# Kernel tuning notes

Hardware: AMD Instinct MI355X
Metric: run time of the kernel (lower is better)

## Reference

```python
import jax, jax.numpy as jnp
import numpy as np

B, N, D, H = 8, 1024, 512, 512  # batch, nodes/graph, input dim, hidden/output dim
NEG_SLOPE = 0.2


def _gatv2_layer(x, src, dst, Wl, bl, Wr, br, a, bias, nseg):
    """PyG GATv2Conv (heads=1, add_self_loops=False, eval mode -> no dropout).
    message j->i: alpha_ij = softmax_i( a . leaky_relu(xl[j] + xr[i]) ); out[i] = sum_j alpha_ij * xl[j] + bias
    """
    xl = x @ Wl + bl              # [nseg, H] source transform
    xr = x @ Wr + br              # [nseg, H] target transform
    e = jax.nn.leaky_relu(xl[src] + xr[dst], NEG_SLOPE) @ a  # [E] raw scores
    m = jax.lax.stop_gradient(jax.ops.segment_max(e, dst, num_segments=nseg))
    ex = jnp.exp(e - m[dst])
    s = jax.ops.segment_sum(ex, dst, num_segments=nseg)
    alpha = ex / s[dst]                                       # segment softmax over incoming edges
    out = jax.ops.segment_sum(alpha[:, None] * xl[src], dst, num_segments=nseg)
    return out + bias


def setup_inputs() -> dict:
    key = jax.random.key(0)
    rng = np.random.RandomState(0)
    # random per-graph adjacency, avg degree ~16; block-diagonal edge extraction
    adj_np = (rng.rand(B, N, N) < (16.0 / N))
    srcs, dsts = [], []
    for b in range(B):  # matches torch.nonzero(big_adj).t(): row=src, col=dst
        r, c = np.nonzero(adj_np[b])
        srcs.append(r + b * N)
        dsts.append(c + b * N)
    edge_index = jnp.asarray(np.stack([np.concatenate(srcs), np.concatenate(dsts)]).astype(np.int32))

    ks = jax.random.split(key, 32)
    def lin(k, fi, fo):
        return (jax.random.normal(k, (fi, fo), jnp.float32) / np.sqrt(fi)).astype(jnp.float32)
    inp = {
        "batch_graph": jax.random.normal(ks[0], (B, N, D), jnp.float32),
        "adj": jnp.asarray(adj_np.astype(np.float32)),
        "edge_index": edge_index,
    }
    dims = [(D, H), (H, H), (H, H)]
    for i, (fi, fo) in enumerate(dims, start=1):
        k = jax.random.split(ks[i], 6)
        inp[f"Wl{i}"] = lin(k[0], fi, fo)
        inp[f"bl{i}"] = jnp.zeros((fo,), jnp.float32)
        inp[f"Wr{i}"] = lin(k[1], fi, fo)
        inp[f"br{i}"] = jnp.zeros((fo,), jnp.float32)
        inp[f"a{i}"] = (jax.random.normal(k[2], (fo,), jnp.float32) / np.sqrt(fo)).astype(jnp.float32)
        inp[f"bias{i}"] = jnp.zeros((fo,), jnp.float32)
    return inp


def reference(batch_graph, adj, edge_index,
              Wl1, bl1, Wr1, br1, a1, bias1,
              Wl2, bl2, Wr2, br2, a2, bias2,
              Wl3, bl3, Wr3, br3, a3, bias3):
    b, n, d = batch_graph.shape
    nseg = b * n
    x = batch_graph.reshape(nseg, d)
    src, dst = edge_index[0], edge_index[1]
    x = _gatv2_layer(x, src, dst, Wl1, bl1, Wr1, br1, a1, bias1, nseg)  # graph_norm = Identity
    x = _gatv2_layer(x, src, dst, Wl2, bl2, Wr2, br2, a2, bias2, nseg)
    x = _gatv2_layer(x, src, dst, Wl3, bl3, Wr3, br3, a3, bias3, nseg)
    return x.reshape(b, n, -1)
```

## Files before the change

kernel.cpp:

```cpp
#include <hip/hip_runtime.h>
#include <math.h>

#define MTOT 8192
#define HD   512

typedef __attribute__((ext_vector_type(8))) short bf16x8;
typedef __attribute__((ext_vector_type(4))) float floatx4;

__device__ inline unsigned short f2bf(float f) {
    unsigned int u = __float_as_uint(f);
    unsigned int r = (u + 0x7FFFu + ((u >> 16) & 1u)) >> 16;
    return (unsigned short)r;
}
__device__ inline float bf2f(unsigned short h) {
    return __uint_as_float(((unsigned int)h) << 16);
}

__device__ inline float wave_sum64(float v) {
    int t;
    t = __builtin_amdgcn_update_dpp(0, __float_as_int(v), 0x121, 0xF, 0xF, true); v += __int_as_float(t);
    t = __builtin_amdgcn_update_dpp(0, __float_as_int(v), 0x122, 0xF, 0xF, true); v += __int_as_float(t);
    t = __builtin_amdgcn_update_dpp(0, __float_as_int(v), 0x124, 0xF, 0xF, true); v += __int_as_float(t);
    t = __builtin_amdgcn_update_dpp(0, __float_as_int(v), 0x128, 0xF, 0xF, true); v += __int_as_float(t);
    v += __shfl_xor(v, 16, 64);
    v += __shfl_xor(v, 32, 64);
    return v;
}


__global__ void count_deg(const int* __restrict__ dst, int* __restrict__ deg, int E) {
    int i = blockIdx.x * 256 + threadIdx.x;
    if (i < E) atomicAdd(&deg[dst[i]], 1);
}

__global__ __launch_bounds__(1024) void scan_offsets(const int* __restrict__ deg,
                                                     int* __restrict__ offs,
                                                     int* __restrict__ cursor) {
    __shared__ int part[1024];
    int tid = threadIdx.x;
    int base = tid * 8;
    int v[8]; int s = 0;
    #pragma unroll
    for (int i = 0; i < 8; ++i) { v[i] = deg[base + i]; s += v[i]; }
    part[tid] = s;
    __syncthreads();
    for (int off = 1; off < 1024; off <<= 1) {
        int t = (tid >= off) ? part[tid - off] : 0;
        __syncthreads();
        part[tid] += t;
        __syncthreads();
    }
    int run = (tid == 0) ? 0 : part[tid - 1];
    #pragma unroll
    for (int i = 0; i < 8; ++i) {
        offs[base + i] = run;
        cursor[base + i] = run;
        run += v[i];
    }
    if (tid == 1023) offs[MTOT] = run;
}

__global__ void scatter_edges(const int* __restrict__ src, const int* __restrict__ dst,
                              int* __restrict__ cursor, int* __restrict__ csr_src, int E) {
    int i = blockIdx.x * 256 + threadIdx.x;
    if (i < E) {
        int p = atomicAdd(&cursor[dst[i]], 1);
        csr_src[p] = src[i];
    }
}


__global__ __launch_bounds__(256) void prep_convert(
    const float* __restrict__ W0, const float* __restrict__ W1,
    const float* __restrict__ W2, const float* __restrict__ W3,
    const float* __restrict__ W4, const float* __restrict__ W5,
    unsigned short* __restrict__ wtbase,
    const float* __restrict__ X,
    unsigned short* __restrict__ Ahi, unsigned short* __restrict__ Alo,
    int* __restrict__ deg)
{
    int z = blockIdx.z;
    if (z == 7) {
        if (blockIdx.x == 0 && blockIdx.y == 0)
            for (int i = threadIdx.x; i < MTOT; i += 256) deg[i] = 0;
        return;
    }
    if (z == 6) {
        int bid = blockIdx.x * 16 + blockIdx.y;
        int t0 = bid * 256 + threadIdx.x;
        #pragma unroll
        for (int it = 0; it < 16; ++it) {
            int i = (t0 + it * 65536) * 4;
            float4 vv = *(const float4*)(X + i);
            ushort4 h, l;
            h.x = f2bf(vv.x); l.x = f2bf(vv.x - bf2f(h.x));
            h.y = f2bf(vv.y); l.y = f2bf(vv.y - bf2f(h.y));
            h.z = f2bf(vv.z); l.z = f2bf(vv.z - bf2f(h.z));
            h.w = f2bf(vv.w); l.w = f2bf(vv.w - bf2f(h.w));
            *(ushort4*)(Ahi + i) = h;
            *(ushort4*)(Alo + i) = l;
        }
        return;
    }
    const float* W = (z == 0) ? W0 : (z == 1) ? W1 : (z == 2) ? W2
                   : (z == 3) ? W3 : (z == 4) ? W4 : W5;
    int L = z >> 1, lr = z & 1;
    const size_t SZ = (size_t)HD * HD;
    unsigned short* Whi = wtbase + (L * 4 + lr * 2) * SZ;
    unsigned short* Wlo = Whi + SZ;

    __shared__ float t[32][33];
    int bx = blockIdx.x * 32;
    int by = blockIdx.y * 32;
    int tx = threadIdx.x & 31, ty = threadIdx.x >> 5;
    for (int i = ty; i < 32; i += 8)
        t[i][tx] = W[(size_t)(by + i) * HD + bx + tx];
    __syncthreads();
    for (int i = ty; i < 32; i += 8) {
        float vv = t[tx][i];
        unsigned short h = f2bf(vv);
        unsigned short l = f2bf(vv - bf2f(h));
        Whi[(size_t)(bx + i) * HD + by + tx] = h;
        Wlo[(size_t)(bx + i) * HD + by + tx] = l;
    }
}


__global__ __launch_bounds__(256) void gemm_mfma_dual(
    const unsigned short* __restrict__ Ahi, const unsigned short* __restrict__ Alo,
    const unsigned short* __restrict__ Bhi_l, const unsigned short* __restrict__ Blo_l,
    const unsigned short* __restrict__ Bhi_r, const unsigned short* __restrict__ Blo_r,
    const float* __restrict__ bias_l, const float* __restrict__ bias_r,
    float* __restrict__ Cl, float* __restrict__ Cr)
{
    int bid = blockIdx.x;
    int virt = (bid & 7) * 64 + (bid >> 3);
    int g  = virt >> 3;
    int q  = virt & 7;
    int bz = q >> 2;
    int bm = g * 128, bn = (q & 3) * 128;

    const unsigned short* Bhi = bz ? Bhi_r : Bhi_l;
    const unsigned short* Blo = bz ? Blo_r : Blo_l;
    const float* bias         = bz ? bias_r : bias_l;
    float* C                  = bz ? Cr : Cl;

    __shared__ __align__(16) unsigned short lds[4 * 128 * 32];

    int tid = threadIdx.x;
    int wave = tid >> 6, lane = tid & 63;

    const unsigned short* gsrc[4] = {Ahi, Alo, Bhi, Blo};
    int rowbase[4] = {bm, bm, bn, bn};

    const unsigned short* gbase =
        gsrc[wave] + (size_t)(rowbase[wave] + (lane >> 2)) * 512 + (lane & 3) * 8;

    floatx4 acc[4][4] = {};

    int wm = wave & 1, wn = wave >> 1;
    int lr = lane & 15, lq = lane >> 4;

    for (int k0 = 0; k0 < 512; k0 += 32) {
        const unsigned short* g2 = gbase + k0;
        #pragma unroll
        for (int rg = 0; rg < 8; ++rg) {
            __builtin_amdgcn_global_load_lds(
                (const __attribute__((address_space(1))) unsigned int*)(g2 + (size_t)rg * 16 * 512),
                (__attribute__((address_space(3))) unsigned int*)(&lds[wave * 4096 + rg * 512]),
                16, 0, 0);
        }
        __syncthreads();

        bf16x8 ah[4], al[4], bh[4], bl_[4];
        #pragma unroll
        for (int i = 0; i < 4; ++i) {
            int mrow = wm * 64 + i * 16 + lr;
            ah[i]  = *(const bf16x8*)&lds[0 * 4096 + mrow * 32 + lq * 8];
            al[i]  = *(const bf16x8*)&lds[1 * 4096 + mrow * 32 + lq * 8];
            int nrow = wn * 64 + i * 16 + lr;
            bh[i]  = *(const bf16x8*)&lds[2 * 4096 + nrow * 32 + lq * 8];
            bl_[i] = *(const bf16x8*)&lds[3 * 4096 + nrow * 32 + lq * 8];
        }
        #pragma unroll
        for (int i = 0; i < 4; ++i)
            #pragma unroll
            for (int j = 0; j < 4; ++j) {
                acc[i][j] = __builtin_amdgcn_mfma_f32_16x16x32_bf16(ah[i], bh[j],  acc[i][j], 0, 0, 0);
                acc[i][j] = __builtin_amdgcn_mfma_f32_16x16x32_bf16(ah[i], bl_[j], acc[i][j], 0, 0, 0);
                acc[i][j] = __builtin_amdgcn_mfma_f32_16x16x32_bf16(al[i], bh[j],  acc[i][j], 0, 0, 0);
            }
        __syncthreads();
    }

    #pragma unroll
    for (int j = 0; j < 4; ++j) {
        int n = bn + wn * 64 + j * 16 + lr;
        float bv = bias[n];
        #pragma unroll
        for (int i = 0; i < 4; ++i) {
            int mbase = bm + wm * 64 + i * 16 + lq * 4;
            #pragma unroll
            for (int r = 0; r < 4; ++r)
                C[(size_t)(mbase + r) * 512 + n] = acc[i][j][r] + bv;
        }
    }
}


__global__ __launch_bounds__(256, 4) void gat_online(
    const float* __restrict__ xl, const float* __restrict__ xr,
    const float* __restrict__ avec, const float* __restrict__ bias,
    const int* __restrict__ offs, const int* __restrict__ csr_src,
    float* __restrict__ out, unsigned short* __restrict__ Ohi,
    unsigned short* __restrict__ Olo, int write_fp32)
{
    int gid = blockIdx.x;
    int wv = threadIdx.x >> 6, lane = threadIdx.x & 63;
    int node = ((gid & 7) << 10) + ((gid >> 3) << 2) + wv;

    int nb = offs[node], ne = offs[node + 1];

    int jc[8];
    int j0 = (nb < ne) ? csr_src[nb] : 0;
    jc[0] = j0;
    #pragma unroll
    for (int k = 1; k < 8; ++k)
        jc[k] = (nb + k < ne) ? csr_src[nb + k] : j0;

    size_t rowoff = (size_t)node * HD + lane * 8;
    float4 r0 = *(const float4*)(xr + rowoff);
    float4 r1 = *(const float4*)(xr + rowoff + 4);
    float4 av0 = *(const float4*)(avec + lane * 8);
    float4 av1 = *(const float4*)(avec + lane * 8 + 4);

    float m = -3.0e38f, s = 0.f;
    float4 acc0 = {0.f, 0.f, 0.f, 0.f}, acc1 = {0.f, 0.f, 0.f, 0.f};

    int p = nb;
    while (p < ne) {
        float4 xa[8], xb[8];
        #pragma unroll
        for (int k = 0; k < 8; ++k) {
            const float* xp = xl + (size_t)jc[k] * HD + lane * 8;
            xa[k] = *(const float4*)xp;
            xb[k] = *(const float4*)(xp + 4);
        }

        int pn = p + 8;
        int jn[8];
        #pragma unroll
        for (int k = 0; k < 8; ++k)
            jn[k] = (pn + k < ne) ? csr_src[pn + k] : jc[0];

        float pe[8];
        #pragma unroll
        for (int k = 0; k < 8; ++k) {
            float t, d = 0.f;
            t = xa[k].x + r0.x; d = fmaf(av0.x, fmaf(0.4f, fabsf(t), 0.6f * t), d);
            t = xa[k].y + r0.y; d = fmaf(av0.y, fmaf(0.4f, fabsf(t), 0.6f * t), d);
            t = xa[k].z + r0.z; d = fmaf(av0.z, fmaf(0.4f, fabsf(t), 0.6f * t), d);
            t = xa[k].w + r0.w; d = fmaf(av0.w, fmaf(0.4f, fabsf(t), 0.6f * t), d);
            t = xb[k].x + r1.x; d = fmaf(av1.x, fmaf(0.4f, fabsf(t), 0.6f * t), d);
            t = xb[k].y + r1.y; d = fmaf(av1.y, fmaf(0.4f, fabsf(t), 0.6f * t), d);
            t = xb[k].z + r1.z; d = fmaf(av1.z, fmaf(0.4f, fabsf(t), 0.6f * t), d);
            t = xb[k].w + r1.w; d = fmaf(av1.w, fmaf(0.4f, fabsf(t), 0.6f * t), d);
            pe[k] = d;
        }

        #pragma unroll
        for (int k = 0; k < 8; ++k) pe[k] = wave_sum64(pe[k]);

        float e[8];
        #pragma unroll
        for (int k = 0; k < 8; ++k) e[k] = (p + k < ne) ? pe[k] : -3.0e38f;

        float bm8 = e[0];
        #pragma unroll
        for (int k = 1; k < 8; ++k) bm8 = fmaxf(bm8, e[k]);

        if (bm8 > m) {
            float sc = __expf(m - bm8);
            s *= sc;
            acc0.x *= sc; acc0.y *= sc; acc0.z *= sc; acc0.w *= sc;
            acc1.x *= sc; acc1.y *= sc; acc1.z *= sc; acc1.w *= sc;
            m = bm8;
        }

        float w[8]; float ws = 0.f;
        #pragma unroll
        for (int k = 0; k < 8; ++k) { w[k] = __expf(e[k] - m); ws += w[k]; }
        s += ws;

        #pragma unroll
        for (int k = 0; k < 8; ++k) {
            acc0.x = fmaf(w[k], xa[k].x, acc0.x);
            acc0.y = fmaf(w[k], xa[k].y, acc0.y);
            acc0.z = fmaf(w[k], xa[k].z, acc0.z);
            acc0.w = fmaf(w[k], xa[k].w, acc0.w);
            acc1.x = fmaf(w[k], xb[k].x, acc1.x);
            acc1.y = fmaf(w[k], xb[k].y, acc1.y);
            acc1.z = fmaf(w[k], xb[k].z, acc1.z);
            acc1.w = fmaf(w[k], xb[k].w, acc1.w);
        }

        #pragma unroll
        for (int k = 0; k < 8; ++k) jc[k] = jn[k];
        p += 8;
    }

    float inv = (s > 0.f) ? 1.f / s : 0.f;
    float4 b0 = *(const float4*)(bias + lane * 8);
    float4 b1 = *(const float4*)(bias + lane * 8 + 4);
    float4 o0, o1;
    o0.x = fmaf(acc0.x, inv, b0.x); o0.y = fmaf(acc0.y, inv, b0.y);
    o0.z = fmaf(acc0.z, inv, b0.z); o0.w = fmaf(acc0.w, inv, b0.w);
    o1.x = fmaf(acc1.x, inv, b1.x); o1.y = fmaf(acc1.y, inv, b1.y);
    o1.z = fmaf(acc1.z, inv, b1.z); o1.w = fmaf(acc1.w, inv, b1.w);

    if (write_fp32) {
        *(float4*)(out + rowoff) = o0;
        *(float4*)(out + rowoff + 4) = o1;
    } else {
        ushort4 h, lo;
        h.x = f2bf(o0.x); lo.x = f2bf(o0.x - bf2f(h.x));
        h.y = f2bf(o0.y); lo.y = f2bf(o0.y - bf2f(h.y));
        h.z = f2bf(o0.z); lo.z = f2bf(o0.z - bf2f(h.z));
        h.w = f2bf(o0.w); lo.w = f2bf(o0.w - bf2f(h.w));
        *(ushort4*)(Ohi + rowoff) = h;
        *(ushort4*)(Olo + rowoff) = lo;
        h.x = f2bf(o1.x); lo.x = f2bf(o1.x - bf2f(h.x));
        h.y = f2bf(o1.y); lo.y = f2bf(o1.y - bf2f(h.y));
        h.z = f2bf(o1.z); lo.z = f2bf(o1.z - bf2f(h.z));
        h.w = f2bf(o1.w); lo.w = f2bf(o1.w - bf2f(h.w));
        *(ushort4*)(Ohi + rowoff + 4) = h;
        *(ushort4*)(Olo + rowoff + 4) = lo;
    }
}


extern "C" void kernel_launch(void* const* d_in, const int* in_sizes, int n_in,
                              void* d_out, int out_size, void* d_ws, size_t ws_size,
                              hipStream_t stream) {
    const float* x0 = (const float*)d_in[0];
    const int* eidx = (const int*)d_in[2];
    int E = in_sizes[2] / 2;
    const int* esrc = eidx;
    const int* edst = eidx + E;

    const float* Wl[3] = {(const float*)d_in[3],  (const float*)d_in[9],  (const float*)d_in[15]};
    const float* bl[3] = {(const float*)d_in[4],  (const float*)d_in[10], (const float*)d_in[16]};
    const float* Wr[3] = {(const float*)d_in[5],  (const float*)d_in[11], (const float*)d_in[17]};
    const float* br[3] = {(const float*)d_in[6],  (const float*)d_in[12], (const float*)d_in[18]};
    const float* av[3] = {(const float*)d_in[7],  (const float*)d_in[13], (const float*)d_in[19]};
    const float* bs[3] = {(const float*)d_in[8],  (const float*)d_in[14], (const float*)d_in[20]};

    char* w = (char*)d_ws;
    unsigned short* Ahi = (unsigned short*)w; w += (size_t)MTOT * HD * 2;
    unsigned short* Alo = (unsigned short*)w; w += (size_t)MTOT * HD * 2;
    unsigned short* wtbase = (unsigned short*)w; w += 12 * (size_t)HD * HD * 2;
    float* xl = (float*)w; w += (size_t)MTOT * HD * 4;
    float* xr = (float*)w; w += (size_t)MTOT * HD * 4;
    int* deg    = (int*)w;
    int* offs   = deg + MTOT;
    int* cursor = offs + MTOT + 8;
    int* csr    = cursor + MTOT;
    const size_t SZ = (size_t)HD * HD;

    prep_convert<<<dim3(16, 16, 8), 256, 0, stream>>>(
        Wl[0], Wr[0], Wl[1], Wr[1], Wl[2], Wr[2], wtbase, x0, Ahi, Alo, deg);
    count_deg<<<(E + 255) / 256, 256, 0, stream>>>(edst, deg, E);
    scan_offsets<<<1, 1024, 0, stream>>>(deg, offs, cursor);
    scatter_edges<<<(E + 255) / 256, 256, 0, stream>>>(esrc, edst, cursor, csr, E);

    for (int L = 0; L < 3; ++L) {
        gemm_mfma_dual<<<512, 256, 0, stream>>>(Ahi, Alo,
            wtbase + (L * 4 + 0) * SZ, wtbase + (L * 4 + 1) * SZ,
            wtbase + (L * 4 + 2) * SZ, wtbase + (L * 4 + 3) * SZ,
            bl[L], br[L], xl, xr);
        int last = (L == 2);
        gat_online<<<MTOT / 4, 256, 0, stream>>>(xl, xr, av[L], bs[L], offs, csr,
                                                 last ? (float*)d_out : nullptr,
                                                 last ? nullptr : Ahi,
                                                 last ? nullptr : Alo,
                                                 last);
    }
}
```

Baseline: 312.5 us.

## Double-buffer edge gathers in GAT aggregation with 4-edge ping-pong batches

Restructures the per-node online-softmax loop into two ping-pong register buffers of 4 edges each. The next batch's xl rows are gathered before the current batch is processed, so gather latency overlaps with compute. The leaky-relu dot product is also split into two accumulators (sum of t and sum of |t|), combined once per edge, which cuts per-element arithmetic. Trade-offs: finer-grained softmax rescaling steps and more live registers, which may hurt occupancy.

```diff
diff --git a/kernel.cpp b/kernel.cpp
--- a/kernel.cpp
+++ b/kernel.cpp
@@ -208,6 +208,55 @@
 }
 
 
+#define DOT8(Xa, Xb, d0, d1)                                              \
+    {                                                                     \
+        float t_;                                                         \
+        t_ = Xa.x + r0.x; d0 = fmaf(av0.x, t_, d0); d1 = fmaf(av0.x, fabsf(t_), d1); \
+        t_ = Xa.y + r0.y; d0 = fmaf(av0.y, t_, d0); d1 = fmaf(av0.y, fabsf(t_), d1); \
+        t_ = Xa.z + r0.z; d0 = fmaf(av0.z, t_, d0); d1 = fmaf(av0.z, fabsf(t_), d1); \
+        t_ = Xa.w + r0.w; d0 = fmaf(av0.w, t_, d0); d1 = fmaf(av0.w, fabsf(t_), d1); \
+        t_ = Xb.x + r1.x; d0 = fmaf(av1.x, t_, d0); d1 = fmaf(av1.x, fabsf(t_), d1); \
+        t_ = Xb.y + r1.y; d0 = fmaf(av1.y, t_, d0); d1 = fmaf(av1.y, fabsf(t_), d1); \
+        t_ = Xb.z + r1.z; d0 = fmaf(av1.z, t_, d0); d1 = fmaf(av1.z, fabsf(t_), d1); \
+        t_ = Xb.w + r1.w; d0 = fmaf(av1.w, t_, d0); d1 = fmaf(av1.w, fabsf(t_), d1); \
+    }
+
+#define PROCESS4(Xa, Xb, q)                                               \
+    {                                                                     \
+        float pe[4];                                                      \
+        _Pragma("unroll")                                                 \
+        for (int k2 = 0; k2 < 4; ++k2) {                                  \
+            float d0 = 0.f, d1 = 0.f;                                     \
+            DOT8(Xa[k2], Xb[k2], d0, d1);                                 \
+            pe[k2] = fmaf(0.6f, d0, 0.4f * d1);                           \
+        }                                                                 \
+        _Pragma("unroll")                                                 \
+        for (int k2 = 0; k2 < 4; ++k2) pe[k2] = wave_sum64(pe[k2]);       \
+        float e0 = pe[0];                                                 \
+        float e1 = ((q) + 1 < ne) ? pe[1] : -3.0e38f;                     \
+        float e2 = ((q) + 2 < ne) ? pe[2] : -3.0e38f;                     \
+        float e3 = ((q) + 3 < ne) ? pe[3] : -3.0e38f;                     \
+        float bm4 = fmaxf(fmaxf(e0, e1), fmaxf(e2, e3));                  \
+        if (bm4 > m) {                                                    \
+            float sc = __expf(m - bm4);                                   \
+            s *= sc;                                                      \
+            acc0.x *= sc; acc0.y *= sc; acc0.z *= sc; acc0.w *= sc;       \
+            acc1.x *= sc; acc1.y *= sc; acc1.z *= sc; acc1.w *= sc;       \
+            m = bm4;                                                      \
+        }                                                                 \
+        float w0 = __expf(e0 - m), w1 = __expf(e1 - m);                   \
+        float w2 = __expf(e2 - m), w3 = __expf(e3 - m);                   \
+        s += (w0 + w1) + (w2 + w3);                                       \
+        acc0.x = fmaf(w0, Xa[0].x, fmaf(w1, Xa[1].x, fmaf(w2, Xa[2].x, fmaf(w3, Xa[3].x, acc0.x)))); \
+        acc0.y = fmaf(w0, Xa[0].y, fmaf(w1, Xa[1].y, fmaf(w2, Xa[2].y, fmaf(w3, Xa[3].y, acc0.y)))); \
+        acc0.z = fmaf(w0, Xa[0].z, fmaf(w1, Xa[1].z, fmaf(w2, Xa[2].z, fmaf(w3, Xa[3].z, acc0.z)))); \
+        acc0.w = fmaf(w0, Xa[0].w, fmaf(w1, Xa[1].w, fmaf(w2, Xa[2].w, fmaf(w3, Xa[3].w, acc0.w)))); \
+        acc1.x = fmaf(w0, Xb[0].x, fmaf(w1, Xb[1].x, fmaf(w2, Xb[2].x, fmaf(w3, Xb[3].x, acc1.x)))); \
+        acc1.y = fmaf(w0, Xb[0].y, fmaf(w1, Xb[1].y, fmaf(w2, Xb[2].y, fmaf(w3, Xb[3].y, acc1.y)))); \
+        acc1.z = fmaf(w0, Xb[0].z, fmaf(w1, Xb[1].z, fmaf(w2, Xb[2].z, fmaf(w3, Xb[3].z, acc1.z)))); \
+        acc1.w = fmaf(w0, Xb[0].w, fmaf(w1, Xb[1].w, fmaf(w2, Xb[2].w, fmaf(w3, Xb[3].w, acc1.w)))); \
+    }
+
 __global__ __launch_bounds__(256, 4) void gat_online(
     const float* __restrict__ xl, const float* __restrict__ xr,
     const float* __restrict__ avec, const float* __restrict__ bias,
@@ -221,97 +270,72 @@
 
     int nb = offs[node], ne = offs[node + 1];
 
-    int jc[8];
+    int jA[4], jB[4];
     int j0 = (nb < ne) ? csr_src[nb] : 0;
-    jc[0] = j0;
-    #pragma unroll
-    for (int k = 1; k < 8; ++k)
-        jc[k] = (nb + k < ne) ? csr_src[nb + k] : j0;
-
-    size_t rowoff = (size_t)node * HD + lane * 8;
+    jA[0] = j0;
+    #pragma unroll
+    for (int k = 1; k < 4; ++k) jA[k] = (nb + k < ne) ? csr_src[nb + k] : j0;
+    #pragma unroll
+    for (int k = 0; k < 4; ++k) jB[k] = (nb + 4 + k < ne) ? csr_src[nb + 4 + k] : j0;
+
+    size_t loff = (size_t)lane * 8;
+    size_t rowoff = (size_t)node * HD + loff;
     float4 r0 = *(const float4*)(xr + rowoff);
     float4 r1 = *(const float4*)(xr + rowoff + 4);
-    float4 av0 = *(const float4*)(avec + lane * 8);
-    float4 av1 = *(const float4*)(avec + lane * 8 + 4);
+    float4 av0 = *(const float4*)(avec + loff);
+    float4 av1 = *(const float4*)(avec + loff + 4);
 
     float m = -3.0e38f, s = 0.f;
     float4 acc0 = {0.f, 0.f, 0.f, 0.f}, acc1 = {0.f, 0.f, 0.f, 0.f};
 
+    float4 Aa[4], Ab[4], Ba[4], Bb[4];
+    #pragma unroll
+    for (int k = 0; k < 4; ++k) {
+        const float* xp = xl + (size_t)jA[k] * HD + loff;
+        Aa[k] = *(const float4*)xp;
+        Ab[k] = *(const float4*)(xp + 4);
+    }
+
     int p = nb;
-    while (p < ne) {
-        float4 xa[8], xb[8];
-        #pragma unroll
-        for (int k = 0; k < 8; ++k) {
-            const float* xp = xl + (size_t)jc[k] * HD + lane * 8;
-            xa[k] = *(const float4*)xp;
-            xb[k] = *(const float4*)(xp + 4);
+    if (p < ne) {
+        for (;;) {
+            #pragma unroll
+            for (int k = 0; k < 4; ++k) {
+                const float* xp = xl + (size_t)jB[k] * HD + loff;
+                Ba[k] = *(const float4*)xp;
+                Bb[k] = *(const float4*)(xp + 4);
+            }
+            {
+                int p2 = p + 8;
+                #pragma unroll
+                for (int k = 0; k < 4; ++k)
+                    jA[k] = (p2 + k < ne) ? csr_src[p2 + k] : j0;
+            }
+            PROCESS4(Aa, Ab, p);
+            p += 4;
+            if (p >= ne) break;
+
+            #pragma unroll
+            for (int k = 0; k < 4; ++k) {
+                const float* xp = xl + (size_t)jA[k] * HD + loff;
+                Aa[k] = *(const float4*)xp;
+                Ab[k] = *(const float4*)(xp + 4);
+            }
+            {
+                int p2 = p + 8;
+                #pragma unroll
+                for (int k = 0; k < 4; ++k)
+                    jB[k] = (p2 + k < ne) ? csr_src[p2 + k] : j0;
+            }
+            PROCESS4(Ba, Bb, p);
+            p += 4;
+            if (p >= ne) break;
         }
-
-        int pn = p + 8;
-        int jn[8];
-        #pragma unroll
-        for (int k = 0; k < 8; ++k)
-            jn[k] = (pn + k < ne) ? csr_src[pn + k] : jc[0];
-
-        float pe[8];
-        #pragma unroll
-        for (int k = 0; k < 8; ++k) {
-            float t, d = 0.f;
-            t = xa[k].x + r0.x; d = fmaf(av0.x, fmaf(0.4f, fabsf(t), 0.6f * t), d);
-            t = xa[k].y + r0.y; d = fmaf(av0.y, fmaf(0.4f, fabsf(t), 0.6f * t), d);
-            t = xa[k].z + r0.z; d = fmaf(av0.z, fmaf(0.4f, fabsf(t), 0.6f * t), d);
-            t = xa[k].w + r0.w; d = fmaf(av0.w, fmaf(0.4f, fabsf(t), 0.6f * t), d);
-            t = xb[k].x + r1.x; d = fmaf(av1.x, fmaf(0.4f, fabsf(t), 0.6f * t), d);
-            t = xb[k].y + r1.y; d = fmaf(av1.y, fmaf(0.4f, fabsf(t), 0.6f * t), d);
-            t = xb[k].z + r1.z; d = fmaf(av1.z, fmaf(0.4f, fabsf(t), 0.6f * t), d);
-            t = xb[k].w + r1.w; d = fmaf(av1.w, fmaf(0.4f, fabsf(t), 0.6f * t), d);
-            pe[k] = d;
-        }
-
-        #pragma unroll
-        for (int k = 0; k < 8; ++k) pe[k] = wave_sum64(pe[k]);
-
-        float e[8];
-        #pragma unroll
-        for (int k = 0; k < 8; ++k) e[k] = (p + k < ne) ? pe[k] : -3.0e38f;
-
-        float bm8 = e[0];
-        #pragma unroll
-        for (int k = 1; k < 8; ++k) bm8 = fmaxf(bm8, e[k]);
-
-        if (bm8 > m) {
-            float sc = __expf(m - bm8);
-            s *= sc;
-            acc0.x *= sc; acc0.y *= sc; acc0.z *= sc; acc0.w *= sc;
-            acc1.x *= sc; acc1.y *= sc; acc1.z *= sc; acc1.w *= sc;
-            m = bm8;
-        }
-
-        float w[8]; float ws = 0.f;
-        #pragma unroll
-        for (int k = 0; k < 8; ++k) { w[k] = __expf(e[k] - m); ws += w[k]; }
-        s += ws;
-
-        #pragma unroll
-        for (int k = 0; k < 8; ++k) {
-            acc0.x = fmaf(w[k], xa[k].x, acc0.x);
-            acc0.y = fmaf(w[k], xa[k].y, acc0.y);
-            acc0.z = fmaf(w[k], xa[k].z, acc0.z);
-            acc0.w = fmaf(w[k], xa[k].w, acc0.w);
-            acc1.x = fmaf(w[k], xb[k].x, acc1.x);
-            acc1.y = fmaf(w[k], xb[k].y, acc1.y);
-            acc1.z = fmaf(w[k], xb[k].z, acc1.z);
-            acc1.w = fmaf(w[k], xb[k].w, acc1.w);
-        }
-
-        #pragma unroll
-        for (int k = 0; k < 8; ++k) jc[k] = jn[k];
-        p += 8;
     }
 
     float inv = (s > 0.f) ? 1.f / s : 0.f;
-    float4 b0 = *(const float4*)(bias + lane * 8);
-    float4 b1 = *(const float4*)(bias + lane * 8 + 4);
+    float4 b0 = *(const float4*)(bias + loff);
+    float4 b1 = *(const float4*)(bias + loff + 4);
     float4 o0, o1;
     o0.x = fmaf(acc0.x, inv, b0.x); o0.y = fmaf(acc0.y, inv, b0.y);
     o0.z = fmaf(acc0.z, inv, b0.z); o0.w = fmaf(acc0.w, inv, b0.w);
```

Measured after the change: 306.4 us. Within noise of the previous version (-1.9%).
